# Performance work log

Hardware: AMD Instinct MI355X
Metric: run time of the kernel (lower is better)

Reference implementation:

```python
import jax, jax.numpy as jnp
import numpy as np

L, B, D, H, DH, M = 1024, 2, 1024, 16, 64, 1024
T = L + M
SCALE = 1.0 / np.sqrt(DH).astype(np.float32)
NEG = -1e30


def _rel_shift(x):
    # x: [L, T, B, H] -- Transformer-XL relative shift along axis 1
    qlen, klen = x.shape[0], x.shape[1]
    zero_pad = jnp.zeros((qlen, 1) + x.shape[2:], x.dtype)
    x_padded = jnp.concatenate([zero_pad, x], axis=1)          # [L, T+1, B, H]
    x_padded = x_padded.reshape((klen + 1, qlen) + x.shape[2:])
    return x_padded[1:].reshape(x.shape)


def setup_inputs() -> dict:
    key = jax.random.key(0)
    ks = jax.random.split(key, 9)
    init = lambda k, shp, s: jax.random.normal(k, shp, jnp.float32) * s
    x = init(ks[0], (L, B, D), 1.0)
    memory = init(ks[1], (M, B, D), 1.0)
    pos_emb = init(ks[2], (T, B, D), 1.0)
    pos_bias_u = init(ks[3], (H, DH), 0.02)
    pos_bias_v = init(ks[4], (H, DH), 0.02)
    s = 1.0 / np.sqrt(D)
    Wq = init(ks[5], (D, H * DH), s)
    Wkv = init(ks[6], (D, 2 * H * DH), s)
    Wrel = init(ks[7], (D, H * DH), s)
    Wo = init(ks[8], (H * DH, D), 1.0 / np.sqrt(H * DH))
    gamma = jnp.ones((D,), jnp.float32)
    beta = jnp.zeros((D,), jnp.float32)
    # causal mask: key position j valid iff j <= i + mem_len
    i = jnp.arange(L)[:, None]
    j = jnp.arange(T)[None, :]
    mask = jnp.broadcast_to((j > i + M)[:, :, None], (L, T, B))
    return dict(x=x, pos_emb=pos_emb, memory=memory, pos_bias_u=pos_bias_u,
                pos_bias_v=pos_bias_v, mask=mask, Wq=Wq, Wkv=Wkv, Wrel=Wrel,
                Wo=Wo, gamma=gamma, beta=beta)


def reference(x, pos_emb, memory, pos_bias_u, pos_bias_v, mask, Wq, Wkv, Wrel, Wo, gamma, beta):
    # vanilla path: memory has same batch size as x
    c = jnp.concatenate([memory, x], axis=0)                   # [T, B, D]
    k, v = jnp.split(c @ Wkv, 2, axis=-1)                      # [T, B, H*DH] each
    q = (x @ Wq).reshape(L, B, H, DH)
    k = k.reshape(T, B, H, DH)
    v = v.reshape(T, B, H, DH)
    r = (pos_emb @ Wrel).reshape(T, B, H, DH)
    AC = jnp.einsum('ibnd,jbnd->ijbn', q + pos_bias_u, k)      # content term
    BD = jnp.einsum('ibnd,jbnd->ijbn', q + pos_bias_v, r)      # position term
    BD = _rel_shift(BD)
    attn_score = (AC + BD) * SCALE                             # [L, T, B, H]
    attn_score = jnp.where(mask[:, :, :, None], NEG, attn_score)
    attn_prob = jax.nn.softmax(attn_score, axis=1)
    attn_matrix = attn_prob.mean(axis=(2, 3))                  # [L, T]
    attn_vec = jnp.einsum('ijbn,jbnd->ibnd', attn_prob, v).reshape(L, B, H * DH)
    attn_out = attn_vec @ Wo                                   # [L, B, D]
    h = x + attn_out
    mu = h.mean(-1, keepdims=True)
    var = h.var(-1, keepdims=True)
    output = (h - mu) / jnp.sqrt(var + 1e-5) * gamma + beta
    return output, attn_matrix
```

## Files before the change

kernel.cpp:

```cpp
#include <hip/hip_runtime.h>
#include <math.h>
#include <stdint.h>

#define L_  1024
#define B_  2
#define D_  1024
#define H_  16
#define DH_ 64
#define M_  1024
#define T_  2048
#define SCALE_ 0.125f
#define SCALE2_ 0.18033688f

typedef unsigned short ushort;
typedef short bf16x8 __attribute__((ext_vector_type(8)));
typedef float f32x4 __attribute__((ext_vector_type(4)));
typedef unsigned short u16x4v __attribute__((ext_vector_type(4)));
typedef unsigned short u16x8v __attribute__((ext_vector_type(8)));

#define MFMA16(a,b,c) __builtin_amdgcn_mfma_f32_16x16x32_bf16(a,b,c,0,0,0)

#if __has_builtin(__builtin_amdgcn_exp2f)
#define EXP2(x) __builtin_amdgcn_exp2f(x)
#else
#define EXP2(x) exp2f(x)
#endif

static __device__ __forceinline__ ushort f2bf(float x) {
    uint32_t u = __float_as_uint(x);
    uint32_t r = (u + 0x7FFFu + ((u >> 16) & 1u)) >> 16;
    return (ushort)r;
}
static __device__ __forceinline__ ushort f2bf_fast(float x) {
    return (ushort)((__float_as_uint(x) + 0x8000u) >> 16);
}
static __device__ __forceinline__ float bf2f(ushort h) {
    return __uint_as_float(((uint32_t)h) << 16);
}
static __device__ __forceinline__ void gl_lds16(const ushort* g, ushort* l) {
    __builtin_amdgcn_global_load_lds(
        (const __attribute__((address_space(1))) void*)g,
        (__attribute__((address_space(3))) void*)l, 16, 0, 0);
}

static __device__ const unsigned char GRP_OF[85] = {
 0,0,0,0, 1,1,1,1, 2,2,2,2, 3,3,3,3,
 4,4,4,4,4, 5,5,5,5,5, 6,6,6,6,6, 7,7,7,7,7, 8,8,8,8,8,
 9,9,9,9,9,9, 10,10,10,10,10,10, 11,11,11,11,11,11,
 12,12,12,12,12,12, 13,13,13,13,13,13,
 14,14,14,14,14,14,14, 15,15,15,15,15,15,15};
static __device__ const unsigned char SLC_OF[85] = {
 0,1,2,3, 0,1,2,3, 0,1,2,3, 0,1,2,3,
 0,1,2,3,4, 0,1,2,3,4, 0,1,2,3,4, 0,1,2,3,4, 0,1,2,3,4,
 0,1,2,3,4,5, 0,1,2,3,4,5, 0,1,2,3,4,5,
 0,1,2,3,4,5, 0,1,2,3,4,5,
 0,1,2,3,4,5,6, 0,1,2,3,4,5,6};
static __device__ const unsigned char NS_OF[16] = {4,4,4,4,5,5,5,5,5,6,6,6,6,6,7,7};

__global__ __launch_bounds__(256) void prep(
    const float* __restrict__ memory, const float* __restrict__ x,
    const float* __restrict__ pos_emb,
    const float* __restrict__ Wq, const float* __restrict__ Wkv,
    const float* __restrict__ Wrel, const float* __restrict__ Wo,
    ushort* __restrict__ cb, ushort* __restrict__ pb,
    ushort* __restrict__ Wqt, ushort* __restrict__ Wkvt,
    ushort* __restrict__ Wrelt, ushort* __restrict__ Wot,
    float* __restrict__ lpart)
{
    __shared__ float t[32][33];
    int tid = threadIdx.x;
    if (blockIdx.x >= 9216) {
        int i = ((blockIdx.x - 9216) * 256 + tid) * 4;
        *(float4*)(lpart + i) = (float4){0.f, 0.f, 0.f, 0.f};
        return;
    }
    if (blockIdx.x < 4096) {
        int idx = (blockIdx.x * 256 + tid) * 8;
        const float* s;
        ushort* d;
        if (idx < 2097152)      { s = memory + idx;              d = cb + idx; }
        else if (idx < 4194304) { s = x + (idx - 2097152);       d = cb + idx; }
        else                    { s = pos_emb + (idx - 4194304); d = pb + (idx - 4194304); }
        float4 a = *(const float4*)(s);
        float4 b = *(const float4*)(s + 4);
        u16x8v o;
        o[0] = f2bf(a.x); o[1] = f2bf(a.y); o[2] = f2bf(a.z); o[3] = f2bf(a.w);
        o[4] = f2bf(b.x); o[5] = f2bf(b.y); o[6] = f2bf(b.z); o[7] = f2bf(b.w);
        *(u16x8v*)d = o;
        return;
    }
    int tb = blockIdx.x - 4096;
    const float* src; ushort* dst; int N;
    if (tb < 1024)      { src = Wq;   dst = Wqt;   N = 1024; }
    else if (tb < 3072) { src = Wkv;  dst = Wkvt;  N = 2048; tb -= 1024; }
    else if (tb < 4096) { src = Wrel; dst = Wrelt; N = 1024; tb -= 3072; }
    else                { src = Wo;   dst = Wot;   N = 1024; tb -= 4096; }
    int k0 = (tb & 31) * 32, n0 = (tb >> 5) * 32;
    int r = tid >> 3, c4 = (tid & 7) * 4;
    float4 v = *(const float4*)(src + (size_t)(k0 + r) * N + n0 + c4);
    t[r][c4 + 0] = v.x; t[r][c4 + 1] = v.y; t[r][c4 + 2] = v.z; t[r][c4 + 3] = v.w;
    __syncthreads();
    u16x4v o;
    o[0] = f2bf(t[c4 + 0][r]); o[1] = f2bf(t[c4 + 1][r]);
    o[2] = f2bf(t[c4 + 2][r]); o[3] = f2bf(t[c4 + 3][r]);
    *(u16x4v*)(dst + (size_t)(n0 + r) * 1024 + k0 + c4) = o;
}

__global__ __launch_bounds__(512) void proj_all(
    const ushort* __restrict__ cb, const ushort* __restrict__ pb,
    const ushort* __restrict__ Wqt, const ushort* __restrict__ Wkvt,
    const ushort* __restrict__ Wrelt,
    const float* __restrict__ bu, const float* __restrict__ bv,
    ushort* __restrict__ quB, ushort* __restrict__ qvB,
    ushort* __restrict__ kbB, ushort* __restrict__ VtB,
    ushort* __restrict__ rbB)
{
    __shared__ ushort Al[3][256 * 32];
    __shared__ ushort Bl[3][256 * 32];
    int lin = blockIdx.x;
    int omode, M0, N0;
    const ushort *A, *Wt;
    if (lin < 32) {
        omode = 0; A = cb + 2097152; Wt = Wqt;
        M0 = (lin & 7) * 256; N0 = (lin >> 3) * 256;
    } else if (lin < 160) {
        omode = 1; A = cb; Wt = Wkvt;
        int l2 = lin - 32;
        M0 = (l2 & 15) * 256; N0 = (l2 >> 4) * 256;
    } else {
        omode = 2; A = pb; Wt = Wrelt;
        int l2 = lin - 160;
        M0 = (l2 & 15) * 256; N0 = (l2 >> 4) * 256;
    }
    int tid = threadIdx.x;
    int wid = tid >> 6, lane = tid & 63, quad = lane >> 4, jl = lane & 15;
    int wr = wid >> 2, wc = wid & 3;
    int srow = lane >> 2;

    f32x4 acc[8][4];
    #pragma unroll
    for (int i = 0; i < 8; ++i)
        #pragma unroll
        for (int j = 0; j < 4; ++j) acc[i][j] = (f32x4){0.f, 0.f, 0.f, 0.f};

    auto stage = [&](int b_, int k0) {
        #pragma unroll
        for (int c = 0; c < 2; ++c) {
            int chunk = wid * 2 + c;
            int r  = chunk * 16 + srow;
            int su = ((lane & 3) - (r >> 1)) & 3;
            gl_lds16(A  + (size_t)(M0 + r) * 1024 + k0 + su * 8,
                     &Al[b_][chunk * 512]);
            gl_lds16(Wt + (size_t)(N0 + r) * 1024 + k0 + su * 8,
                     &Bl[b_][chunk * 512]);
        }
        __builtin_amdgcn_sched_barrier(0);
    };

#define PROJ_STEP(IDX, BUF, SBUF, WAITN)                                    \
    {                                                                       \
        asm volatile("s_waitcnt vmcnt(" #WAITN ")" ::: "memory");           \
        __builtin_amdgcn_sched_barrier(0);                                  \
        __builtin_amdgcn_s_barrier();                                       \
        if ((IDX) + 2 < 32) stage((SBUF), ((IDX) + 2) * 32);                \
        bf16x8 af[8], bfr[4];                                               \
        _Pragma("unroll")                                                   \
        for (int mt = 0; mt < 8; ++mt) {                                    \
            int ra = wr * 128 + mt * 16 + jl;                               \
            int u  = (quad + (ra >> 1)) & 3;                                \
            af[mt] = *(const bf16x8*)&Al[(BUF)][ra * 32 + u * 8];           \
        }                                                                   \
        _Pragma("unroll")                                                   \
        for (int nt = 0; nt < 4; ++nt) {                                    \
            int rb_ = wc * 64 + nt * 16 + jl;                               \
            int u   = (quad + (rb_ >> 1)) & 3;                              \
            bfr[nt] = *(const bf16x8*)&Bl[(BUF)][rb_ * 32 + u * 8];         \
        }                                                                   \
        _Pragma("unroll")                                                   \
        for (int mt = 0; mt < 8; ++mt)                                      \
            _Pragma("unroll")                                               \
            for (int nt = 0; nt < 4; ++nt)                                  \
                acc[mt][nt] = MFMA16(af[mt], bfr[nt], acc[mt][nt]);         \
    }

    stage(0, 0);
    stage(1, 32);

    #pragma unroll 1
    for (int i3 = 0; i3 < 30; i3 += 3) {
        PROJ_STEP(i3 + 0, 0, 2, 4);
        PROJ_STEP(i3 + 1, 1, 0, 4);
        PROJ_STEP(i3 + 2, 2, 1, 4);
    }
    PROJ_STEP(30, 0, 2, 4);
    PROJ_STEP(31, 1, 0, 0);
#undef PROJ_STEP

    if (omode == 0) {
        #pragma unroll
        for (int mt = 0; mt < 8; ++mt)
            #pragma unroll
            for (int nt = 0; nt < 4; ++nt)
                #pragma unroll
                for (int r = 0; r < 4; ++r) {
                    int gm = M0 + wr * 128 + mt * 16 + quad * 4 + r;
                    int gn = N0 + wc * 64 + nt * 16 + jl;
                    float v = acc[mt][nt][r];
                    int l = gm >> 1, b = gm & 1;
                    int h = gn >> 6, d = gn & 63;
                    size_t o = ((size_t)((b << 4) | h) * 1024 + l) * 64 + d;
                    quB[o] = f2bf(v + bu[gn]);
                    qvB[o] = f2bf(v + bv[gn]);
                }
    } else if (omode == 2) {
        #pragma unroll
        for (int mt = 0; mt < 8; ++mt)
            #pragma unroll
            for (int nt = 0; nt < 4; ++nt)
                #pragma unroll
                for (int r = 0; r < 4; ++r) {
                    int gm = M0 + wr * 128 + mt * 16 + quad * 4 + r;
                    int gn = N0 + wc * 64 + nt * 16 + jl;
                    int t2 = gm >> 1, b = gm & 1;
                    int h = gn >> 6, d = gn & 63;
                    rbB[((size_t)((b << 4) | h) * 2048 + t2) * 64 + d] =
                        f2bf(acc[mt][nt][r]);
                }
    } else if (N0 < 1024) {
        #pragma unroll
        for (int mt = 0; mt < 8; ++mt)
            #pragma unroll
            for (int nt = 0; nt < 4; ++nt)
                #pragma unroll
                for (int r = 0; r < 4; ++r) {
                    int gm = M0 + wr * 128 + mt * 16 + quad * 4 + r;
                    int gn = N0 + wc * 64 + nt * 16 + jl;
                    int t2 = gm >> 1, b = gm & 1;
                    int h = gn >> 6, d = gn & 63;
                    kbB[((size_t)((b << 4) | h) * 2048 + t2) * 64 + d] =
                        f2bf(acc[mt][nt][r]);
                }
    } else {
        #pragma unroll
        for (int nt = 0; nt < 4; ++nt) {
            int nn = (N0 + wc * 64 + nt * 16 + jl) & 1023;
            int h = nn >> 6, d = nn & 63;
            #pragma unroll
            for (int g = 0; g < 2; ++g)
                #pragma unroll
                for (int b = 0; b < 2; ++b) {
                    u16x8v pk;
                    #pragma unroll
                    for (int e = 0; e < 8; ++e)
                        pk[e] = f2bf(acc[2 * (e & 3) + g][nt][b + 2 * (e >> 2)]);
                    size_t tp = (size_t)(M0 >> 1) + wr * 64 + g * 32 + quad * 8;
                    *(u16x8v*)(VtB + ((size_t)((b << 4) | h) * 64 + d) * 2048 + tp) = pk;
                }
        }
    }
}

__global__ __launch_bounds__(256) void attn_score(
    const ushort* __restrict__ qu, const ushort* __restrict__ qv,
    const ushort* __restrict__ kb, const ushort* __restrict__ rb,
    float* __restrict__ lpart, ushort* __restrict__ AMw)
{
    __shared__ ushort Kl[2][64 * 64];
    __shared__ ushort Rl[2][128 * 64];

    int tid = threadIdx.x, wid = tid >> 6, lane = tid & 63;
    int quad = lane >> 4, jl = lane & 15, jx = jl & 7;

    int lin  = blockIdx.x;
    int xcd  = lin & 7;
    int rest = lin >> 3;
    int bh   = (xcd << 2) | (rest & 3);
    int sidx = rest >> 2;
    int grp  = GRP_OF[sidx];
    int slc  = SLC_OF[sidx];
    int nc   = 17 + grp;
    int ns   = NS_OF[grp];
    int cb_  = slc * nc / ns;
    int ce_  = (slc + 1) * nc / ns;
    int it   = grp * 4 + wid;
    int i0w  = it * 16;
    int irow = i0w + quad * 4;

    const ushort* kp  = kb + (size_t)bh * 2048 * 64;
    const ushort* rp  = rb + (size_t)bh * 2048 * 64;
    const ushort* qup = qu + (size_t)bh * 1024 * 64;
    const ushort* qvp = qv + (size_t)bh * 1024 * 64;

    bf16x8 quA[2], qvA[2];
    quA[0] = *(const bf16x8*)(qup + (size_t)(i0w + jl) * 64 + quad * 8);
    quA[1] = *(const bf16x8*)(qup + (size_t)(i0w + jl) * 64 + 32 + quad * 8);
    qvA[0] = *(const bf16x8*)(qvp + (size_t)(i0w + jl) * 64 + quad * 8);
    qvA[1] = *(const bf16x8*)(qvp + (size_t)(i0w + jl) * 64 + 32 + quad * 8);

    ushort* prow0 = AMw + ((size_t)irow * 32 + bh) * 2048 + jl * 4;

    int lrow = lane >> 3;
    int scol = ((lane & 7) ^ lrow) * 8;

    f32x4 z = (f32x4){0.f, 0.f, 0.f, 0.f};
    float lsum[4] = {0.f, 0.f, 0.f, 0.f};

    auto stage = [&](int b_, int c) {
        int j0n = c * 64;
        int rbase = 960 + j0n - grp * 64;
        ushort* KB = &Kl[b_][0];
        ushort* RB = &Rl[b_][0];
        #pragma unroll
        for (int q = 0; q < 6; ++q) {
            int rgn = wid * 6 + q;
            if (rgn < 8) {
                int row = rgn * 8 + lrow;
                gl_lds16(kp + (size_t)(j0n + row) * 64 + scol, KB + rgn * 512);
            } else {
                int row = (rgn - 8) * 8 + lrow;
                int rg = rbase + row;
                rg = rg > 2047 ? 2047 : rg;
                gl_lds16(rp + (size_t)rg * 64 + scol, RB + (rgn - 8) * 512);
            }
        }
        __builtin_amdgcn_sched_barrier(0);
    };

    int buf = 0;
    stage(0, cb_);
    asm volatile("s_waitcnt vmcnt(0)" ::: "memory");
    __builtin_amdgcn_sched_barrier(0);
    __builtin_amdgcn_s_barrier();

    for (int c = cb_; c < ce_; ++c) {
        if (c + 1 < ce_) stage(buf ^ 1, c + 1);
        int j0 = c * 64;
        int d0 = 1008 + j0 - i0w;
        bool interior = (j0 + 63 <= i0w + M_) && (d0 + 79 <= 2047);
        const ushort* KB = &Kl[buf][0];
        const ushort* RB = &Rl[buf][0];
        f32x4 ac[4];
        #pragma unroll
        for (int su = 0; su < 4; ++su) {
            int row = su * 16 + jl;
            int s0 = (quad ^ jx) * 8;
            bf16x8 k0v = *(const bf16x8*)&KB[row * 64 + s0];
            bf16x8 k1v = *(const bf16x8*)&KB[row * 64 + (s0 ^ 32)];
            f32x4 t = MFMA16(quA[0], k0v, z);
            ac[su] = MFMA16(quA[1], k1v, t);
        }
        int ob = 48 - wid * 16 + jl;
        f32x4 bt[5];
        #pragma unroll
        for (int nt = 0; nt < 5; ++nt) {
            int o = ob + nt * 16;
            int s0 = (quad ^ jx) * 8;
            bf16x8 r0 = *(const bf16x8*)&RB[o * 64 + s0];
            bf16x8 r1 = *(const bf16x8*)&RB[o * 64 + (s0 ^ 32)];
            f32x4 t = MFMA16(qvA[0], r0, z);
            bt[nt] = MFMA16(qvA[1], r1, t);
        }
        float bs[4][5];
        #pragma unroll
        for (int r = 0; r < 4; ++r) {
            int ii = quad * 4 + r;
            int src = (quad << 4) | ((jl + 15 - ii) & 15);
            #pragma unroll
            for (int nt = 0; nt < 5; ++nt) bs[r][nt] = __shfl(bt[nt][r], src);
        }
        if (interior) {
            #pragma unroll
            for (int r = 0; r < 4; ++r) {
                int ii = quad * 4 + r;
                bool hi = (jl > ii);
                u16x4v ps;
                #pragma unroll
                for (int su = 0; su < 4; ++su) {
                    float bd = hi ? bs[r][su + 1] : bs[r][su];
                    float p = EXP2(fminf((ac[su][r] + bd) * SCALE2_, 86.f));
                    lsum[r] += p;
                    ps[su] = f2bf_fast(p);
                }
                *(u16x4v*)(prow0 + (size_t)r * 65536 + j0) = ps;
            }
        } else {
            #pragma unroll
            for (int r = 0; r < 4; ++r) {
                int ii = quad * 4 + r;
                bool hi = (jl > ii);
                u16x4v ps;
                #pragma unroll
                for (int su = 0; su < 4; ++su) {
                    float bd = hi ? bs[r][su + 1] : bs[r][su];
                    float sv = (ac[su][r] + bd) * SCALE2_;
                    int j = j0 + su * 16 + jl;
                    float p = (j <= irow + r + M_) ? EXP2(fminf(sv, 86.f)) : 0.f;
                    lsum[r] += p;
                    ps[su] = f2bf_fast(p);
                }
                *(u16x4v*)(prow0 + (size_t)r * 65536 + j0) = ps;
            }
        }
        asm volatile("s_waitcnt vmcnt(4)" ::: "memory");
        __builtin_amdgcn_sched_barrier(0);
        __builtin_amdgcn_s_barrier();
        buf ^= 1;
    }

    #pragma unroll
    for (int r = 0; r < 4; ++r) {
        #pragma unroll
        for (int off = 1; off < 16; off <<= 1) lsum[r] += __shfl_xor(lsum[r], off);
        if (jl == 0) atomicAdd(&lpart[(size_t)bh * 1024 + irow + r], lsum[r]);
    }
}

__global__ __launch_bounds__(256) void pv_gemm(
    const ushort* __restrict__ P, const ushort* __restrict__ Vt,
    const float* __restrict__ lpart,
    ushort* __restrict__ OvecB, float* __restrict__ linvs)
{
    __shared__ ushort Al[64][40];
    __shared__ ushort Bl[64][40];
    int tid = threadIdx.x;
    int lin  = blockIdx.x;
    int xcd  = lin & 7;
    int rest = lin >> 3;
    int bh   = (xcd << 2) | (rest & 3);
    int mt   = rest >> 2;
    int M0   = mt * 64;
    int wid = tid >> 6, lane = tid & 63, quad = lane >> 4, jl = lane & 15;
    int m0w = (wid >> 1) * 32, n0w = (wid & 1) * 32;
    int sr = tid >> 2, sc = (tid & 3) * 8;

    const ushort* Bp = Vt + (size_t)bh * 64 * 2048;
    int kend = (17 + mt) * 64;

    f32x4 acc[2][2];
    #pragma unroll
    for (int i = 0; i < 2; ++i)
        #pragma unroll
        for (int j = 0; j < 2; ++j) acc[i][j] = (f32x4){0.f, 0.f, 0.f, 0.f};

    for (int k0 = 0; k0 < kend; k0 += 32) {
        *(u16x8v*)&Al[sr][sc] =
            *(const u16x8v*)(P + ((size_t)(M0 + sr) * 32 + bh) * 2048 + k0 + sc);
        *(u16x8v*)&Bl[sr][sc] = *(const u16x8v*)(Bp + (size_t)sr * 2048 + k0 + sc);
        __syncthreads();
        bf16x8 a0 = *(const bf16x8*)&Al[m0w + jl][quad * 8];
        bf16x8 a1 = *(const bf16x8*)&Al[m0w + 16 + jl][quad * 8];
        bf16x8 b0 = *(const bf16x8*)&Bl[n0w + jl][quad * 8];
        bf16x8 b1 = *(const bf16x8*)&Bl[n0w + 16 + jl][quad * 8];
        acc[0][0] = MFMA16(a0, b0, acc[0][0]);
        acc[0][1] = MFMA16(a0, b1, acc[0][1]);
        acc[1][0] = MFMA16(a1, b0, acc[1][0]);
        acc[1][1] = MFMA16(a1, b1, acc[1][1]);
        __syncthreads();
    }

    int b = bh >> 4, h = bh & 15;
    #pragma unroll
    for (int ms = 0; ms < 2; ++ms)
        #pragma unroll
        for (int r = 0; r < 4; ++r) {
            int gi = M0 + m0w + 16 * ms + quad * 4 + r;
            float linv = 1.f / lpart[(size_t)bh * 1024 + gi];
            #pragma unroll
            for (int ns = 0; ns < 2; ++ns) {
                int gd = n0w + 16 * ns + jl;
                OvecB[(size_t)(gi * 2 + b) * 1024 + h * 64 + gd] =
                    f2bf(acc[ms][ns][r] * linv);
            }
            if (n0w == 0 && jl == 0)
                linvs[(size_t)gi * 32 + bh] = linv * 0.03125f;
        }
}

__global__ __launch_bounds__(256) void tail_fused(
    const ushort* __restrict__ A, const ushort* __restrict__ Wt,
    const float* __restrict__ resid, float* __restrict__ outF,
    const ushort* __restrict__ AMw, const float* __restrict__ linvs,
    float* __restrict__ AM)
{
    __shared__ ushort Al[64][40];
    __shared__ ushort Bl[64][40];
    int tid = threadIdx.x;
    int lin = blockIdx.x;
    if (lin >= 512) {
        __shared__ float lv[32];
        __shared__ float jbuf[2048];
        int i = lin - 512;
        if (tid < 32) lv[tid] = linvs[(size_t)i * 32 + tid];
        __syncthreads();
        int k0 = tid * 8;
        int jmax = i + M_;
        float acc[8];
        #pragma unroll
        for (int e = 0; e < 8; ++e) acc[e] = 0.f;
        if ((k0 & ~63) <= jmax) {
            const ushort* base = AMw + (size_t)i * 65536;
            for (int p = 0; p < 32; ++p) {
                float l = lv[p];
                u16x8v v = *(const u16x8v*)(base + (size_t)p * 2048 + k0);
                #pragma unroll
                for (int e = 0; e < 8; ++e) acc[e] += bf2f(v[e]) * l;
            }
        }
        #pragma unroll
        for (int e = 0; e < 8; ++e) {
            int kp = k0 + e;
            int j  = (kp & ~63) | ((kp & 3) << 4) | ((kp >> 2) & 15);
            jbuf[j] = acc[e];
        }
        __syncthreads();
        int j0 = tid * 8;
        float4 o0, o1;
        o0.x = (j0 + 0 <= jmax) ? jbuf[j0 + 0] : 0.f;
        o0.y = (j0 + 1 <= jmax) ? jbuf[j0 + 1] : 0.f;
        o0.z = (j0 + 2 <= jmax) ? jbuf[j0 + 2] : 0.f;
        o0.w = (j0 + 3 <= jmax) ? jbuf[j0 + 3] : 0.f;
        o1.x = (j0 + 4 <= jmax) ? jbuf[j0 + 4] : 0.f;
        o1.y = (j0 + 5 <= jmax) ? jbuf[j0 + 5] : 0.f;
        o1.z = (j0 + 6 <= jmax) ? jbuf[j0 + 6] : 0.f;
        o1.w = (j0 + 7 <= jmax) ? jbuf[j0 + 7] : 0.f;
        *(float4*)(AM + (size_t)i * 2048 + j0) = o0;
        *(float4*)(AM + (size_t)i * 2048 + j0 + 4) = o1;
        return;
    }
    int M0 = (lin & 31) * 64, N0 = (lin >> 5) * 64;
    int wid = tid >> 6, lane = tid & 63, quad = lane >> 4, jl = lane & 15;
    int m0w = (wid >> 1) * 32, n0w = (wid & 1) * 32;
    int sr = tid >> 2, sc = (tid & 3) * 8;

    f32x4 acc[2][2];
    #pragma unroll
    for (int i = 0; i < 2; ++i)
        #pragma unroll
        for (int j = 0; j < 2; ++j) acc[i][j] = (f32x4){0.f, 0.f, 0.f, 0.f};

    for (int k0 = 0; k0 < 1024; k0 += 32) {
        *(u16x8v*)&Al[sr][sc] = *(const u16x8v*)(A  + (size_t)(M0 + sr) * 1024 + k0 + sc);
        *(u16x8v*)&Bl[sr][sc] = *(const u16x8v*)(Wt + (size_t)(N0 + sr) * 1024 + k0 + sc);
        __syncthreads();
        bf16x8 a0 = *(const bf16x8*)&Al[m0w + jl][quad * 8];
        bf16x8 a1 = *(const bf16x8*)&Al[m0w + 16 + jl][quad * 8];
        bf16x8 b0 = *(const bf16x8*)&Bl[n0w + jl][quad * 8];
        bf16x8 b1 = *(const bf16x8*)&Bl[n0w + 16 + jl][quad * 8];
        acc[0][0] = MFMA16(a0, b0, acc[0][0]);
        acc[0][1] = MFMA16(a0, b1, acc[0][1]);
        acc[1][0] = MFMA16(a1, b0, acc[1][0]);
        acc[1][1] = MFMA16(a1, b1, acc[1][1]);
        __syncthreads();
    }

    #pragma unroll
    for (int ms = 0; ms < 2; ++ms)
        #pragma unroll
        for (int ns = 0; ns < 2; ++ns)
            #pragma unroll
            for (int r = 0; r < 4; ++r) {
                int gm = M0 + m0w + 16 * ms + quad * 4 + r;
                int gn = N0 + n0w + 16 * ns + jl;
                outF[(size_t)gm * 1024 + gn] =
                    acc[ms][ns][r] + resid[(size_t)gm * 1024 + gn];
            }
}

__global__ __launch_bounds__(256) void ln_kernel(
    const float* __restrict__ hbuf,
    const float* __restrict__ gamma, const float* __restrict__ beta,
    float* __restrict__ out)
{
    __shared__ float rs[4], rss[4];
    int row = blockIdx.x;
    int tid = threadIdx.x;
    const float* hp = hbuf + (size_t)row * 1024;
    float4 h4 = *(const float4*)(hp + (tid << 2));
    float s = h4.x + h4.y + h4.z + h4.w;
    float ss = h4.x * h4.x + h4.y * h4.y + h4.z * h4.z + h4.w * h4.w;
    #pragma unroll
    for (int o = 32; o > 0; o >>= 1) {
        s  += __shfl_down(s, o);
        ss += __shfl_down(ss, o);
    }
    if ((tid & 63) == 0) { rs[tid >> 6] = s; rss[tid >> 6] = ss; }
    __syncthreads();
    float tot  = rs[0] + rs[1] + rs[2] + rs[3];
    float tots = rss[0] + rss[1] + rss[2] + rss[3];
    float mu = tot * (1.f / 1024.f);
    float var = tots * (1.f / 1024.f) - mu * mu;
    float rstd = rsqrtf(var + 1e-5f);
    float4 g4 = *(const float4*)(gamma + (tid << 2));
    float4 b4 = *(const float4*)(beta + (tid << 2));
    float4 o4;
    o4.x = (h4.x - mu) * rstd * g4.x + b4.x;
    o4.y = (h4.y - mu) * rstd * g4.y + b4.y;
    o4.z = (h4.z - mu) * rstd * g4.z + b4.z;
    o4.w = (h4.w - mu) * rstd * g4.w + b4.w;
    *(float4*)(out + (size_t)row * 1024 + (tid << 2)) = o4;
}

extern "C" void kernel_launch(void* const* d_in, const int* in_sizes, int n_in,
                              void* d_out, int out_size, void* d_ws, size_t ws_size,
                              hipStream_t stream) {
    const float* x       = (const float*)d_in[0];
    const float* pos_emb = (const float*)d_in[1];
    const float* memory  = (const float*)d_in[2];
    const float* bu      = (const float*)d_in[3];
    const float* bv      = (const float*)d_in[4];
    const float* Wq      = (const float*)d_in[6];
    const float* Wkv     = (const float*)d_in[7];
    const float* Wrel    = (const float*)d_in[8];
    const float* Wo      = (const float*)d_in[9];
    const float* gamma   = (const float*)d_in[10];
    const float* beta    = (const float*)d_in[11];

    float* out = (float*)d_out;
    float* AM  = out + (size_t)2097152;

    ushort* cb    = (ushort*)d_ws;
    ushort* pb    = cb    + 4194304;
    ushort* Wqt   = pb    + 4194304;
    ushort* Wkvt  = Wqt   + 1048576;
    ushort* Wrelt = Wkvt  + 2097152;
    ushort* Wot   = Wrelt + 1048576;
    ushort* quB   = Wot   + 1048576;
    ushort* qvB   = quB   + 2097152;
    ushort* kbB   = qvB   + 2097152;
    ushort* VtB   = kbB   + 4194304;
    ushort* rbB   = VtB   + 4194304;
    ushort* OvecB = rbB   + 4194304;
    float*  hbuf  = (float*)(OvecB + 2097152);
    float*  lpart = hbuf  + 2097152;
    float*  linvs = lpart + 32768;
    ushort* AMw   = (ushort*)(linvs + 32768);

    dim3 blk(256);
    prep<<<9248, blk, 0, stream>>>(memory, x, pos_emb, Wq, Wkv, Wrel, Wo,
                                   cb, pb, Wqt, Wkvt, Wrelt, Wot, lpart);
    proj_all<<<224, dim3(512), 0, stream>>>(cb, pb, Wqt, Wkvt, Wrelt, bu, bv,
                                            quB, qvB, kbB, VtB, rbB);
    attn_score<<<dim3(2720), blk, 0, stream>>>(quB, qvB, kbB, rbB, lpart, AMw);
    pv_gemm<<<dim3(512), blk, 0, stream>>>(AMw, VtB, lpart, OvecB, linvs);
    tail_fused<<<dim3(1536), blk, 0, stream>>>(OvecB, Wot, x, hbuf,
                                               AMw, linvs, AM);
    ln_kernel<<<2048, blk, 0, stream>>>(hbuf, gamma, beta, out);
}
```

Before: 279.5 us.

## Enlarge PV and output-projection GEMM tiles with double-buffered direct-to-LDS loads

pv_gemm now processes 128 query rows per block, with each wave covering the full 64-wide head dimension. Each wave stops its MFMA work at its own causal bound, while the shared loads continue to the block maximum. The Wo GEMM in tail_fused moves to 128x128 tiles with 4x4 MFMA accumulators per wave. It loads through double-buffered, swizzled global-to-LDS loads so fetches overlap compute. The goal is more reuse per loaded tile and less loop and barrier overhead, at the cost of fewer blocks, more registers, and some redundant causal-tile loads.

```diff
diff --git a/kernel.cpp b/kernel.cpp
--- a/kernel.cpp
+++ b/kernel.cpp
@@ -420,41 +420,53 @@
     const float* __restrict__ lpart,
     ushort* __restrict__ OvecB, float* __restrict__ linvs)
 {
-    __shared__ ushort Al[64][40];
+    __shared__ ushort Al[128][40];
     __shared__ ushort Bl[64][40];
     int tid = threadIdx.x;
     int lin  = blockIdx.x;
     int xcd  = lin & 7;
     int rest = lin >> 3;
     int bh   = (xcd << 2) | (rest & 3);
-    int mt   = rest >> 2;
-    int M0   = mt * 64;
+    int st   = rest >> 2;
+    int M0   = st * 128;
     int wid = tid >> 6, lane = tid & 63, quad = lane >> 4, jl = lane & 15;
-    int m0w = (wid >> 1) * 32, n0w = (wid & 1) * 32;
+    int mt   = st * 2 + (wid >> 1);
+    int m0w  = (wid >> 1) * 64 + (wid & 1) * 32;
+    int kend_w   = (17 + mt) * 64;
+    int kend_max = (18 + st * 2) * 64;
+
+    const ushort* Bp = Vt + (size_t)bh * 64 * 2048;
     int sr = tid >> 2, sc = (tid & 3) * 8;
 
-    const ushort* Bp = Vt + (size_t)bh * 64 * 2048;
-    int kend = (17 + mt) * 64;
-
-    f32x4 acc[2][2];
+    f32x4 acc[2][4];
     #pragma unroll
     for (int i = 0; i < 2; ++i)
         #pragma unroll
-        for (int j = 0; j < 2; ++j) acc[i][j] = (f32x4){0.f, 0.f, 0.f, 0.f};
-
-    for (int k0 = 0; k0 < kend; k0 += 32) {
+        for (int j = 0; j < 4; ++j) acc[i][j] = (f32x4){0.f, 0.f, 0.f, 0.f};
+
+    for (int k0 = 0; k0 < kend_max; k0 += 32) {
         *(u16x8v*)&Al[sr][sc] =
             *(const u16x8v*)(P + ((size_t)(M0 + sr) * 32 + bh) * 2048 + k0 + sc);
+        *(u16x8v*)&Al[sr + 64][sc] =
+            *(const u16x8v*)(P + ((size_t)(M0 + sr + 64) * 32 + bh) * 2048 + k0 + sc);
         *(u16x8v*)&Bl[sr][sc] = *(const u16x8v*)(Bp + (size_t)sr * 2048 + k0 + sc);
         __syncthreads();
-        bf16x8 a0 = *(const bf16x8*)&Al[m0w + jl][quad * 8];
-        bf16x8 a1 = *(const bf16x8*)&Al[m0w + 16 + jl][quad * 8];
-        bf16x8 b0 = *(const bf16x8*)&Bl[n0w + jl][quad * 8];
-        bf16x8 b1 = *(const bf16x8*)&Bl[n0w + 16 + jl][quad * 8];
-        acc[0][0] = MFMA16(a0, b0, acc[0][0]);
-        acc[0][1] = MFMA16(a0, b1, acc[0][1]);
-        acc[1][0] = MFMA16(a1, b0, acc[1][0]);
-        acc[1][1] = MFMA16(a1, b1, acc[1][1]);
+        if (k0 < kend_w) {
+            bf16x8 a0 = *(const bf16x8*)&Al[m0w + jl][quad * 8];
+            bf16x8 a1 = *(const bf16x8*)&Al[m0w + 16 + jl][quad * 8];
+            bf16x8 b0 = *(const bf16x8*)&Bl[jl][quad * 8];
+            bf16x8 b1 = *(const bf16x8*)&Bl[16 + jl][quad * 8];
+            bf16x8 b2 = *(const bf16x8*)&Bl[32 + jl][quad * 8];
+            bf16x8 b3 = *(const bf16x8*)&Bl[48 + jl][quad * 8];
+            acc[0][0] = MFMA16(a0, b0, acc[0][0]);
+            acc[0][1] = MFMA16(a0, b1, acc[0][1]);
+            acc[0][2] = MFMA16(a0, b2, acc[0][2]);
+            acc[0][3] = MFMA16(a0, b3, acc[0][3]);
+            acc[1][0] = MFMA16(a1, b0, acc[1][0]);
+            acc[1][1] = MFMA16(a1, b1, acc[1][1]);
+            acc[1][2] = MFMA16(a1, b2, acc[1][2]);
+            acc[1][3] = MFMA16(a1, b3, acc[1][3]);
+        }
         __syncthreads();
     }
 
@@ -466,12 +478,12 @@
             int gi = M0 + m0w + 16 * ms + quad * 4 + r;
             float linv = 1.f / lpart[(size_t)bh * 1024 + gi];
             #pragma unroll
-            for (int ns = 0; ns < 2; ++ns) {
-                int gd = n0w + 16 * ns + jl;
+            for (int ns = 0; ns < 4; ++ns) {
+                int gd = 16 * ns + jl;
                 OvecB[(size_t)(gi * 2 + b) * 1024 + h * 64 + gd] =
                     f2bf(acc[ms][ns][r] * linv);
             }
-            if (n0w == 0 && jl == 0)
+            if (jl == 0)
                 linvs[(size_t)gi * 32 + bh] = linv * 0.03125f;
         }
 }
@@ -482,14 +494,14 @@
     const ushort* __restrict__ AMw, const float* __restrict__ linvs,
     float* __restrict__ AM)
 {
-    __shared__ ushort Al[64][40];
-    __shared__ ushort Bl[64][40];
+    __shared__ ushort Al[2][128 * 32];
+    __shared__ ushort Bl[2][128 * 32];
     int tid = threadIdx.x;
     int lin = blockIdx.x;
-    if (lin >= 512) {
+    if (lin >= 128) {
         __shared__ float lv[32];
         __shared__ float jbuf[2048];
-        int i = lin - 512;
+        int i = lin - 128;
         if (tid < 32) lv[tid] = linvs[(size_t)i * 32 + tid];
         __syncthreads();
         int k0 = tid * 8;
@@ -527,42 +539,72 @@
         *(float4*)(AM + (size_t)i * 2048 + j0 + 4) = o1;
         return;
     }
-    int M0 = (lin & 31) * 64, N0 = (lin >> 5) * 64;
+    int M0 = (lin & 15) * 128, N0 = (lin >> 4) * 128;
     int wid = tid >> 6, lane = tid & 63, quad = lane >> 4, jl = lane & 15;
-    int m0w = (wid >> 1) * 32, n0w = (wid & 1) * 32;
-    int sr = tid >> 2, sc = (tid & 3) * 8;
-
-    f32x4 acc[2][2];
+    int wr = wid >> 1, wc = wid & 1;
+    int srow = lane >> 2;
+
+    f32x4 acc[4][4];
     #pragma unroll
-    for (int i = 0; i < 2; ++i)
-        #pragma unroll
-        for (int j = 0; j < 2; ++j) acc[i][j] = (f32x4){0.f, 0.f, 0.f, 0.f};
+    for (int i = 0; i < 4; ++i)
+        #pragma unroll
+        for (int j = 0; j < 4; ++j) acc[i][j] = (f32x4){0.f, 0.f, 0.f, 0.f};
+
+    auto stage = [&](int b_, int k0) {
+        #pragma unroll
+        for (int c = 0; c < 2; ++c) {
+            int r  = wid * 32 + c * 16 + srow;
+            int su = ((lane & 3) - (r >> 1)) & 3;
+            gl_lds16(A  + (size_t)(M0 + r) * 1024 + k0 + su * 8,
+                     &Al[b_][wid * 1024 + c * 512]);
+            gl_lds16(Wt + (size_t)(N0 + r) * 1024 + k0 + su * 8,
+                     &Bl[b_][wid * 1024 + c * 512]);
+        }
+        __builtin_amdgcn_sched_barrier(0);
+    };
+
+    int buf = 0;
+    stage(0, 0);
+    asm volatile("s_waitcnt vmcnt(0)" ::: "memory");
+    __builtin_amdgcn_sched_barrier(0);
+    __builtin_amdgcn_s_barrier();
 
     for (int k0 = 0; k0 < 1024; k0 += 32) {
-        *(u16x8v*)&Al[sr][sc] = *(const u16x8v*)(A  + (size_t)(M0 + sr) * 1024 + k0 + sc);
-        *(u16x8v*)&Bl[sr][sc] = *(const u16x8v*)(Wt + (size_t)(N0 + sr) * 1024 + k0 + sc);
-        __syncthreads();
-        bf16x8 a0 = *(const bf16x8*)&Al[m0w + jl][quad * 8];
-        bf16x8 a1 = *(const bf16x8*)&Al[m0w + 16 + jl][quad * 8];
-        bf16x8 b0 = *(const bf16x8*)&Bl[n0w + jl][quad * 8];
-        bf16x8 b1 = *(const bf16x8*)&Bl[n0w + 16 + jl][quad * 8];
-        acc[0][0] = MFMA16(a0, b0, acc[0][0]);
-        acc[0][1] = MFMA16(a0, b1, acc[0][1]);
-        acc[1][0] = MFMA16(a1, b0, acc[1][0]);
-        acc[1][1] = MFMA16(a1, b1, acc[1][1]);
-        __syncthreads();
+        if (k0 + 32 < 1024) stage(buf ^ 1, k0 + 32);
+        bf16x8 af[4], bfr[4];
+        #pragma unroll
+        for (int mt = 0; mt < 4; ++mt) {
+            int ra = wr * 64 + mt * 16 + jl;
+            int u  = (quad + (ra >> 1)) & 3;
+            af[mt] = *(const bf16x8*)&Al[buf][ra * 32 + u * 8];
+        }
+        #pragma unroll
+        for (int nt = 0; nt < 4; ++nt) {
+            int rb_ = wc * 64 + nt * 16 + jl;
+            int u   = (quad + (rb_ >> 1)) & 3;
+            bfr[nt] = *(const bf16x8*)&Bl[buf][rb_ * 32 + u * 8];
+        }
+        #pragma unroll
+        for (int mt = 0; mt < 4; ++mt)
+            #pragma unroll
+            for (int nt = 0; nt < 4; ++nt)
+                acc[mt][nt] = MFMA16(af[mt], bfr[nt], acc[mt][nt]);
+        asm volatile("s_waitcnt vmcnt(0)" ::: "memory");
+        __builtin_amdgcn_sched_barrier(0);
+        __builtin_amdgcn_s_barrier();
+        buf ^= 1;
     }
 
     #pragma unroll
-    for (int ms = 0; ms < 2; ++ms)
-        #pragma unroll
-        for (int ns = 0; ns < 2; ++ns)
+    for (int mt = 0; mt < 4; ++mt)
+        #pragma unroll
+        for (int nt = 0; nt < 4; ++nt)
             #pragma unroll
             for (int r = 0; r < 4; ++r) {
-                int gm = M0 + m0w + 16 * ms + quad * 4 + r;
-                int gn = N0 + n0w + 16 * ns + jl;
+                int gm = M0 + wr * 64 + mt * 16 + quad * 4 + r;
+                int gn = N0 + wc * 64 + nt * 16 + jl;
                 outF[(size_t)gm * 1024 + gn] =
-                    acc[ms][ns][r] + resid[(size_t)gm * 1024 + gn];
+                    acc[mt][nt][r] + resid[(size_t)gm * 1024 + gn];
             }
 }
 
@@ -641,8 +683,8 @@
     proj_all<<<224, dim3(512), 0, stream>>>(cb, pb, Wqt, Wkvt, Wrelt, bu, bv,
                                             quB, qvB, kbB, VtB, rbB);
     attn_score<<<dim3(2720), blk, 0, stream>>>(quB, qvB, kbB, rbB, lpart, AMw);
-    pv_gemm<<<dim3(512), blk, 0, stream>>>(AMw, VtB, lpart, OvecB, linvs);
-    tail_fused<<<dim3(1536), blk, 0, stream>>>(OvecB, Wot, x, hbuf,
+    pv_gemm<<<dim3(256), blk, 0, stream>>>(AMw, VtB, lpart, OvecB, linvs);
+    tail_fused<<<dim3(1152), blk, 0, stream>>>(OvecB, Wot, x, hbuf,
                                                AMw, linvs, AM);
     ln_kernel<<<2048, blk, 0, stream>>>(hbuf, gamma, beta, out);
 }
```

Result: slower. 291.0 us (+4.1%).
